# Kernel optimization log

Hardware: AMD Instinct MI355X
Metric: run time of the kernel (lower is better)

The kernel has to match this reference:

```python
import jax, jax.numpy as jnp
import numpy as np
import math

B, S, D_IN, D_OUT, H = 2, 2048, 1024, 1024, 16
HD = D_OUT // H


def setup_inputs() -> dict:
    key = jax.random.key(0)
    ks = jax.random.split(key, 6)
    scale = 0.02
    return {
        "x": jax.random.normal(ks[0], (B, S, D_IN), dtype=jnp.float32),
        "Wq": jax.random.normal(ks[1], (D_IN, D_OUT), dtype=jnp.float32) * scale,
        "Wk": jax.random.normal(ks[2], (D_IN, D_OUT), dtype=jnp.float32) * scale,
        "Wv": jax.random.normal(ks[3], (D_IN, D_OUT), dtype=jnp.float32) * scale,
        "Wo": jax.random.normal(ks[4], (D_OUT, D_OUT), dtype=jnp.float32) * scale,
        "bo": jax.random.normal(ks[5], (D_OUT,), dtype=jnp.float32) * scale,
    }


def reference(x, Wq, Wk, Wv, Wo, bo):
    b, n, _ = x.shape
    # project and split heads -> [b, h, n, hd]
    q = (x @ Wq).reshape(b, n, H, HD).transpose(0, 2, 1, 3)
    k = (x @ Wk).reshape(b, n, H, HD).transpose(0, 2, 1, 3)
    v = (x @ Wv).reshape(b, n, H, HD).transpose(0, 2, 1, 3)
    # materialized [b, h, n, n] scores with causal mask (as in original)
    scores = jnp.einsum('bhqd,bhkd->bhqk', q, k)
    causal = jnp.tril(jnp.ones((n, n), dtype=bool))  # True = keep
    scores = jnp.where(causal, scores, -jnp.inf)
    attn = jax.nn.softmax(scores / math.sqrt(HD), axis=-1)
    ctx = jnp.einsum('bhqk,bhkd->bhqd', attn, v)
    ctx = ctx.transpose(0, 2, 1, 3).reshape(b, n, D_OUT)
    return ctx @ Wo + bo
```

## Files before the change

### kernel.cpp

```cpp
#include <hip/hip_runtime.h>
#include <hip/hip_bf16.h>
#include <math.h>

typedef __bf16 v8bf __attribute__((ext_vector_type(8)));
typedef float  v4f  __attribute__((ext_vector_type(4)));
typedef unsigned short u16;

static_assert(sizeof(v8bf) == 16, "v8bf must be 16B");

__device__ __forceinline__ u16 f2bf(float f) {
  __hip_bfloat16 h = __float2bfloat16(f);
  return *reinterpret_cast<u16*>(&h);
}
__device__ __forceinline__ v4f mfma16(v8bf a, v8bf b, v4f c) {
  return __builtin_amdgcn_mfma_f32_16x16x32_bf16(a, b, c, 0, 0, 0);
}
__device__ __forceinline__ void async16(const u16* g, u16* l) {
  __builtin_amdgcn_global_load_lds(
      (__attribute__((address_space(1))) void*)(void*)g,
      (__attribute__((address_space(3))) void*)l, 16, 0, 0);
}

__global__ void convert_x(const float* __restrict__ x, u16* __restrict__ xb) {
  int i = (blockIdx.x * 256 + threadIdx.x) * 4;
  float4 v = *(const float4*)(x + i);
  ushort4 o;
  o.x = f2bf(v.x); o.y = f2bf(v.y); o.z = f2bf(v.z); o.w = f2bf(v.w);
  *(ushort4*)(xb + i) = o;
}

__global__ void transpose_w(const float* __restrict__ Wq, const float* __restrict__ Wk,
                            const float* __restrict__ Wv, const float* __restrict__ Wo,
                            u16* __restrict__ Wt) {
  __shared__ float tile[32][33];
  const float* src = (blockIdx.z == 0) ? Wq : (blockIdx.z == 1) ? Wk : (blockIdx.z == 2) ? Wv : Wo;
  int k0 = blockIdx.x * 32, n0 = blockIdx.y * 32;
  int tx = threadIdx.x, ty = threadIdx.y;
  tile[ty][tx] = src[(size_t)(k0 + ty) * 1024 + n0 + tx];
  __syncthreads();
  Wt[(size_t)(blockIdx.z * 1024 + n0 + ty) * 1024 + k0 + tx] = f2bf(tile[tx][ty]);
}

__global__ void transpose_v(const u16* __restrict__ qkv, u16* __restrict__ Vt) {
  __shared__ u16 tile[32][33];
  int b = blockIdx.z;
  int s0 = blockIdx.x * 32, d0 = blockIdx.y * 32;
  int tx = threadIdx.x, ty = threadIdx.y;
  tile[ty][tx] = qkv[(size_t)(b * 2048 + s0 + ty) * 3072 + 2048 + d0 + tx];
  __syncthreads();
  Vt[(size_t)(b * 1024 + d0 + ty) * 2048 + s0 + tx] = tile[tx][ty];
}

__device__ __forceinline__ void gemm_core(const u16* __restrict__ A, const u16* __restrict__ Bt,
                                          u16* sA, u16* sB, v4f acc[4][4], int bm, int bn) {
  const int t = threadIdx.x;
  const int w = t >> 6, l = t & 63;
  const int quad = l >> 4, low = l & 15;
  const int wm = (w & 1) * 64, wn = (w >> 1) * 64;
  const int rowA = bm * 128 + w * 32 + (l >> 2);
  const int rowB = bn * 128 + w * 32 + (l >> 2);
  const int col8 = (l & 3) * 8;
  u16* la = sA + w * 1024;
  u16* lb = sB + w * 1024;

  for (int kb = 0; kb < 1024; kb += 32) {
    async16(A + (size_t)rowA * 1024 + kb + col8, la);
    async16(A + (size_t)(rowA + 16) * 1024 + kb + col8, la + 512);
    async16(Bt + (size_t)rowB * 1024 + kb + col8, lb);
    async16(Bt + (size_t)(rowB + 16) * 1024 + kb + col8, lb + 512);
    __syncthreads();
    v8bf af[4], bfr[4];
#pragma unroll
    for (int i = 0; i < 4; i++)
      af[i] = *(const v8bf*)(sA + (wm + i * 16 + low) * 32 + quad * 8);
#pragma unroll
    for (int j = 0; j < 4; j++)
      bfr[j] = *(const v8bf*)(sB + (wn + j * 16 + low) * 32 + quad * 8);
#pragma unroll
    for (int i = 0; i < 4; i++)
#pragma unroll
      for (int j = 0; j < 4; j++)
        acc[i][j] = mfma16(af[i], bfr[j], acc[i][j]);
    __syncthreads();
  }
}

__global__ __launch_bounds__(256) void gemm_qkv(const u16* __restrict__ xb,
                                                const u16* __restrict__ Wt,
                                                u16* __restrict__ qkv) {
  __shared__ __align__(16) u16 sA[128 * 32];
  __shared__ __align__(16) u16 sB[128 * 32];
  v4f acc[4][4] = {};
  const int bm = blockIdx.x, bn = blockIdx.y;
  gemm_core(xb, Wt, sA, sB, acc, bm, bn);
  const int t = threadIdx.x, w = t >> 6, l = t & 63, quad = l >> 4, low = l & 15;
  const int wm = (w & 1) * 64, wn = (w >> 1) * 64;
#pragma unroll
  for (int i = 0; i < 4; i++) {
    int m0 = bm * 128 + wm + i * 16 + quad * 4;
#pragma unroll
    for (int j = 0; j < 4; j++) {
      int n = bn * 128 + wn + j * 16 + low;
      float qsc = (n < 1024) ? 0.18033688011112042f : 1.0f;
#pragma unroll
      for (int r = 0; r < 4; r++)
        qkv[(size_t)(m0 + r) * 3072 + n] = f2bf(acc[i][j][r] * qsc);
    }
  }
}

__global__ __launch_bounds__(256) void gemm_out(const u16* __restrict__ ctx,
                                                const u16* __restrict__ Wt,
                                                const float* __restrict__ bo,
                                                float* __restrict__ out) {
  __shared__ __align__(16) u16 sA[128 * 32];
  __shared__ __align__(16) u16 sB[64 * 32];
  const u16* Bt = Wt + (size_t)3072 * 1024;
  v4f acc[4][2] = {};
  const int bm = blockIdx.x, bn = blockIdx.y;
  const int t = threadIdx.x, w = t >> 6, l = t & 63, quad = l >> 4, low = l & 15;
  const int wm = (w & 1) * 64, wn = (w >> 1) * 32;
  const int rowA = bm * 128 + w * 32 + (l >> 2);
  const int rowB = bn * 64 + w * 16 + (l >> 2);
  const int col8 = (l & 3) * 8;
  u16* la = sA + w * 1024;
  u16* lb = sB + w * 512;

  for (int kb = 0; kb < 1024; kb += 32) {
    async16(ctx + (size_t)rowA * 1024 + kb + col8, la);
    async16(ctx + (size_t)(rowA + 16) * 1024 + kb + col8, la + 512);
    async16(Bt + (size_t)rowB * 1024 + kb + col8, lb);
    __syncthreads();
    v8bf af[4], bfr[2];
#pragma unroll
    for (int i = 0; i < 4; i++)
      af[i] = *(const v8bf*)(sA + (wm + i * 16 + low) * 32 + quad * 8);
#pragma unroll
    for (int j = 0; j < 2; j++)
      bfr[j] = *(const v8bf*)(sB + (wn + j * 16 + low) * 32 + quad * 8);
#pragma unroll
    for (int i = 0; i < 4; i++)
#pragma unroll
      for (int j = 0; j < 2; j++)
        acc[i][j] = mfma16(af[i], bfr[j], acc[i][j]);
    __syncthreads();
  }
#pragma unroll
  for (int i = 0; i < 4; i++) {
    int m0 = bm * 128 + wm + i * 16 + quad * 4;
#pragma unroll
    for (int j = 0; j < 2; j++) {
      int n = bn * 64 + wn + j * 16 + low;
      float bias = bo[n];
#pragma unroll
      for (int r = 0; r < 4; r++)
        out[(size_t)(m0 + r) * 1024 + n] = acc[i][j][r] + bias;
    }
  }
}

__global__ __launch_bounds__(256) void attn(const u16* __restrict__ qkv,
                                            const u16* __restrict__ Vt,
                                            u16* __restrict__ ctx) {
  __shared__ __align__(16) u16 sK[2][4096];
  __shared__ __align__(16) u16 sV[2][4096];
  __shared__ __align__(16) u16 pS[4][16][72];
  const int t = threadIdx.x, w = t >> 6, l = t & 63, quad = l >> 4, low = l & 15;
  const int h = blockIdx.x, tile = 31 - blockIdx.y, b = blockIdx.z;
  const int qw = tile * 64 + w * 16;
  const int nkt = tile + 1;

  const u16* kbase = qkv + (size_t)(b * 2048) * 3072 + 1024 + h * 64;
  const u16* vbase = Vt + (size_t)(b * 1024 + h * 64) * 2048;

  const int srow = l >> 3;
  const int cg = (l & 7) ^ srow;

  const u16* qrow = qkv + (size_t)(b * 2048 + qw + low) * 3072 + h * 64;
  v8bf qa0 = *(const v8bf*)(qrow + quad * 8);
  v8bf qa1 = *(const v8bf*)(qrow + 32 + quad * 8);

  float li[4] = {0.f, 0.f, 0.f, 0.f};
  v4f o[4] = {};

  {
    const u16* kg = kbase + (size_t)(w * 8 + srow) * 3072 + cg * 8;
    async16(kg, &sK[0][w * 512]);
    async16(kg + (size_t)32 * 3072, &sK[0][2048 + w * 512]);
    const u16* vg = vbase + (size_t)(w * 8 + srow) * 2048 + cg * 8;
    async16(vg, &sV[0][w * 512]);
    async16(vg + (size_t)32 * 2048, &sV[0][2048 + w * 512]);
  }

  for (int it = 0; it < nkt; it++) {
    __syncthreads();
    const int kb = it * 64;
    const int cur = it & 1;
    if (it + 1 < nkt) {
      const int nb = (it + 1) & 1;
      const u16* kg = kbase + (size_t)(kb + 64 + w * 8 + srow) * 3072 + cg * 8;
      async16(kg, &sK[nb][w * 512]);
      async16(kg + (size_t)32 * 3072, &sK[nb][2048 + w * 512]);
      const u16* vg = vbase + (size_t)(w * 8 + srow) * 2048 + kb + 64 + cg * 8;
      async16(vg, &sV[nb][w * 512]);
      async16(vg + (size_t)32 * 2048, &sV[nb][2048 + w * 512]);
    }

    v4f s[4] = {};
#pragma unroll
    for (int cf = 0; cf < 4; cf++) {
      const int key = cf * 16 + low;
#pragma unroll
      for (int ks = 0; ks < 2; ks++) {
        const int chunk = ks * 4 + quad;
        v8bf kf = *(const v8bf*)(&sK[cur][key * 64 + ((chunk ^ (key & 7)) * 8)]);
        s[cf] = mfma16(ks == 0 ? qa0 : qa1, kf, s[cf]);
      }
    }

    const bool diag = (it == nkt - 1);
#pragma unroll
    for (int r = 0; r < 4; r++) {
      const int qr = qw + quad * 4 + r;
#pragma unroll
      for (int cf = 0; cf < 4; cf++) {
        float e = __builtin_amdgcn_exp2f(s[cf][r]);
        if (diag && (kb + cf * 16 + low > qr)) e = 0.f;
        li[r] += e;
        pS[w][quad * 4 + r][cf * 16 + low] = f2bf(e);
      }
    }

    v8bf pa0 = *(const v8bf*)(&pS[w][low][quad * 8]);
    v8bf pa1 = *(const v8bf*)(&pS[w][low][32 + quad * 8]);
#pragma unroll
    for (int df = 0; df < 4; df++) {
      const int d = df * 16 + low;
      v8bf vf0 = *(const v8bf*)(&sV[cur][d * 64 + ((quad ^ (d & 7)) * 8)]);
      v8bf vf1 = *(const v8bf*)(&sV[cur][d * 64 + (((4 + quad) ^ (d & 7)) * 8)]);
      o[df] = mfma16(pa0, vf0, o[df]);
      o[df] = mfma16(pa1, vf1, o[df]);
    }
  }

#pragma unroll
  for (int off = 1; off < 16; off <<= 1)
#pragma unroll
    for (int r = 0; r < 4; r++)
      li[r] += __shfl_xor(li[r], off);

#pragma unroll
  for (int r = 0; r < 4; r++) {
    float inv = 1.f / li[r];
    int row = b * 2048 + qw + quad * 4 + r;
#pragma unroll
    for (int df = 0; df < 4; df++)
      ctx[(size_t)row * 1024 + h * 64 + df * 16 + low] = f2bf(o[df][r] * inv);
  }
}

extern "C" void kernel_launch(void* const* d_in, const int* in_sizes, int n_in,
                              void* d_out, int out_size, void* d_ws, size_t ws_size,
                              hipStream_t stream) {
  const float* x  = (const float*)d_in[0];
  const float* Wq = (const float*)d_in[1];
  const float* Wk = (const float*)d_in[2];
  const float* Wv = (const float*)d_in[3];
  const float* Wo = (const float*)d_in[4];
  const float* bo = (const float*)d_in[5];
  float* out = (float*)d_out;

  char* ws = (char*)d_ws;
  u16* xb  = (u16*)(ws);
  u16* Wt  = (u16*)(ws + 8ull * 1024 * 1024);
  u16* qkv = (u16*)(ws + 16ull * 1024 * 1024);
  u16* Vt  = (u16*)(ws + 40ull * 1024 * 1024);
  u16* ctx = (u16*)(ws + 48ull * 1024 * 1024);

  convert_x<<<dim3(4096, 1, 1), dim3(256, 1, 1), 0, stream>>>(x, xb);
  transpose_w<<<dim3(32, 32, 4), dim3(32, 32, 1), 0, stream>>>(Wq, Wk, Wv, Wo, Wt);
  gemm_qkv<<<dim3(32, 24, 1), dim3(256, 1, 1), 0, stream>>>(xb, Wt, qkv);
  transpose_v<<<dim3(64, 32, 2), dim3(32, 32, 1), 0, stream>>>(qkv, Vt);
  attn<<<dim3(16, 32, 2), dim3(256, 1, 1), 0, stream>>>(qkv, Vt, ctx);
  gemm_out<<<dim3(32, 16, 1), dim3(256, 1, 1), 0, stream>>>(ctx, Wt, bo, out);
}
```

Measured before the change: 185.4 us.

## Fuse prep kernels, write V transposed from QKV GEMM, enlarge attention query tile

Merges the x conversion and weight transposes into one prep launch. The QKV GEMM epilogue now writes separate Q, K and transposed V buffers, which removes the transpose_v kernel and a round-trip of V through memory. The attention kernel gives each wave 32 query rows (128 per block) so each K/V tile loaded into shared memory is reused twice as much, and waves skip key tiles above their causal limit. The cost is fewer blocks, which may leave CUs idle, more registers per thread, and strided column writes for Vt that are poorly coalesced.

```diff
diff --git a/kernel.cpp b/kernel.cpp
--- a/kernel.cpp
+++ b/kernel.cpp
@@ -21,34 +21,26 @@
       (__attribute__((address_space(3))) void*)l, 16, 0, 0);
 }
 
-__global__ void convert_x(const float* __restrict__ x, u16* __restrict__ xb) {
-  int i = (blockIdx.x * 256 + threadIdx.x) * 4;
-  float4 v = *(const float4*)(x + i);
-  ushort4 o;
-  o.x = f2bf(v.x); o.y = f2bf(v.y); o.z = f2bf(v.z); o.w = f2bf(v.w);
-  *(ushort4*)(xb + i) = o;
-}
-
-__global__ void transpose_w(const float* __restrict__ Wq, const float* __restrict__ Wk,
-                            const float* __restrict__ Wv, const float* __restrict__ Wo,
-                            u16* __restrict__ Wt) {
+__global__ void prep(const float* __restrict__ x, const float* __restrict__ Wq,
+                     const float* __restrict__ Wk, const float* __restrict__ Wv,
+                     const float* __restrict__ Wo, u16* __restrict__ Wt,
+                     u16* __restrict__ xb) {
+  int tx = threadIdx.x, ty = threadIdx.y;
+  if (blockIdx.z == 4) {
+    int bid = blockIdx.y * 32 + blockIdx.x;
+    int i = (bid * 1024 + ty * 32 + tx) * 4;
+    float4 v = *(const float4*)(x + i);
+    ushort4 o;
+    o.x = f2bf(v.x); o.y = f2bf(v.y); o.z = f2bf(v.z); o.w = f2bf(v.w);
+    *(ushort4*)(xb + i) = o;
+    return;
+  }
   __shared__ float tile[32][33];
   const float* src = (blockIdx.z == 0) ? Wq : (blockIdx.z == 1) ? Wk : (blockIdx.z == 2) ? Wv : Wo;
   int k0 = blockIdx.x * 32, n0 = blockIdx.y * 32;
-  int tx = threadIdx.x, ty = threadIdx.y;
   tile[ty][tx] = src[(size_t)(k0 + ty) * 1024 + n0 + tx];
   __syncthreads();
   Wt[(size_t)(blockIdx.z * 1024 + n0 + ty) * 1024 + k0 + tx] = f2bf(tile[tx][ty]);
-}
-
-__global__ void transpose_v(const u16* __restrict__ qkv, u16* __restrict__ Vt) {
-  __shared__ u16 tile[32][33];
-  int b = blockIdx.z;
-  int s0 = blockIdx.x * 32, d0 = blockIdx.y * 32;
-  int tx = threadIdx.x, ty = threadIdx.y;
-  tile[ty][tx] = qkv[(size_t)(b * 2048 + s0 + ty) * 3072 + 2048 + d0 + tx];
-  __syncthreads();
-  Vt[(size_t)(b * 1024 + d0 + ty) * 2048 + s0 + tx] = tile[tx][ty];
 }
 
 __device__ __forceinline__ void gemm_core(const u16* __restrict__ A, const u16* __restrict__ Bt,
@@ -87,7 +79,9 @@
 
 __global__ __launch_bounds__(256) void gemm_qkv(const u16* __restrict__ xb,
                                                 const u16* __restrict__ Wt,
-                                                u16* __restrict__ qkv) {
+                                                u16* __restrict__ Qb,
+                                                u16* __restrict__ Kb,
+                                                u16* __restrict__ Vt) {
   __shared__ __align__(16) u16 sA[128 * 32];
   __shared__ __align__(16) u16 sB[128 * 32];
   v4f acc[4][4] = {};
@@ -95,16 +89,28 @@
   gemm_core(xb, Wt, sA, sB, acc, bm, bn);
   const int t = threadIdx.x, w = t >> 6, l = t & 63, quad = l >> 4, low = l & 15;
   const int wm = (w & 1) * 64, wn = (w >> 1) * 64;
+  const int zone = (bn * 128) >> 10;
+  const float qsc = (zone == 0) ? 0.18033688011112042f : 1.0f;
 #pragma unroll
   for (int i = 0; i < 4; i++) {
     int m0 = bm * 128 + wm + i * 16 + quad * 4;
 #pragma unroll
     for (int j = 0; j < 4; j++) {
-      int n = bn * 128 + wn + j * 16 + low;
-      float qsc = (n < 1024) ? 0.18033688011112042f : 1.0f;
-#pragma unroll
-      for (int r = 0; r < 4; r++)
-        qkv[(size_t)(m0 + r) * 3072 + n] = f2bf(acc[i][j][r] * qsc);
+      int nn = (bn * 128 + wn + j * 16 + low) & 1023;
+      if (zone == 0) {
+#pragma unroll
+        for (int r = 0; r < 4; r++)
+          Qb[(size_t)(m0 + r) * 1024 + nn] = f2bf(acc[i][j][r] * qsc);
+      } else if (zone == 1) {
+#pragma unroll
+        for (int r = 0; r < 4; r++)
+          Kb[(size_t)(m0 + r) * 1024 + nn] = f2bf(acc[i][j][r]);
+      } else {
+        int bb = m0 >> 11, s = m0 & 2047;
+#pragma unroll
+        for (int r = 0; r < 4; r++)
+          Vt[(size_t)(bb * 1024 + nn) * 2048 + s + r] = f2bf(acc[i][j][r]);
+      }
     }
   }
 }
@@ -159,34 +165,39 @@
   }
 }
 
-__global__ __launch_bounds__(256) void attn(const u16* __restrict__ qkv,
+__global__ __launch_bounds__(256) void attn(const u16* __restrict__ Qb,
+                                            const u16* __restrict__ Kb,
                                             const u16* __restrict__ Vt,
                                             u16* __restrict__ ctx) {
   __shared__ __align__(16) u16 sK[2][4096];
   __shared__ __align__(16) u16 sV[2][4096];
-  __shared__ __align__(16) u16 pS[4][16][72];
+  __shared__ __align__(16) u16 pS[4][32][72];
   const int t = threadIdx.x, w = t >> 6, l = t & 63, quad = l >> 4, low = l & 15;
-  const int h = blockIdx.x, tile = 31 - blockIdx.y, b = blockIdx.z;
-  const int qw = tile * 64 + w * 16;
-  const int nkt = tile + 1;
-
-  const u16* kbase = qkv + (size_t)(b * 2048) * 3072 + 1024 + h * 64;
+  const int h = blockIdx.x, tile = 15 - blockIdx.y, b = blockIdx.z;
+  const int qw = tile * 128 + w * 32;
+  const int nkt = 2 * tile + 2;
+
+  const u16* kbase = Kb + (size_t)(b * 2048) * 1024 + h * 64;
   const u16* vbase = Vt + (size_t)(b * 1024 + h * 64) * 2048;
 
   const int srow = l >> 3;
   const int cg = (l & 7) ^ srow;
 
-  const u16* qrow = qkv + (size_t)(b * 2048 + qw + low) * 3072 + h * 64;
-  v8bf qa0 = *(const v8bf*)(qrow + quad * 8);
-  v8bf qa1 = *(const v8bf*)(qrow + 32 + quad * 8);
-
-  float li[4] = {0.f, 0.f, 0.f, 0.f};
-  v4f o[4] = {};
+  v8bf qa[2][2];
+#pragma unroll
+  for (int mi = 0; mi < 2; mi++) {
+    const u16* qrow = Qb + (size_t)(b * 2048 + qw + mi * 16 + low) * 1024 + h * 64;
+    qa[mi][0] = *(const v8bf*)(qrow + quad * 8);
+    qa[mi][1] = *(const v8bf*)(qrow + 32 + quad * 8);
+  }
+
+  float li[2][4] = {};
+  v4f o[2][4] = {};
 
   {
-    const u16* kg = kbase + (size_t)(w * 8 + srow) * 3072 + cg * 8;
+    const u16* kg = kbase + (size_t)(w * 8 + srow) * 1024 + cg * 8;
     async16(kg, &sK[0][w * 512]);
-    async16(kg + (size_t)32 * 3072, &sK[0][2048 + w * 512]);
+    async16(kg + (size_t)32 * 1024, &sK[0][2048 + w * 512]);
     const u16* vg = vbase + (size_t)(w * 8 + srow) * 2048 + cg * 8;
     async16(vg, &sV[0][w * 512]);
     async16(vg + (size_t)32 * 2048, &sV[0][2048 + w * 512]);
@@ -198,65 +209,82 @@
     const int cur = it & 1;
     if (it + 1 < nkt) {
       const int nb = (it + 1) & 1;
-      const u16* kg = kbase + (size_t)(kb + 64 + w * 8 + srow) * 3072 + cg * 8;
+      const u16* kg = kbase + (size_t)(kb + 64 + w * 8 + srow) * 1024 + cg * 8;
       async16(kg, &sK[nb][w * 512]);
-      async16(kg + (size_t)32 * 3072, &sK[nb][2048 + w * 512]);
+      async16(kg + (size_t)32 * 1024, &sK[nb][2048 + w * 512]);
       const u16* vg = vbase + (size_t)(w * 8 + srow) * 2048 + kb + 64 + cg * 8;
       async16(vg, &sV[nb][w * 512]);
       async16(vg + (size_t)32 * 2048, &sV[nb][2048 + w * 512]);
     }
 
-    v4f s[4] = {};
-#pragma unroll
-    for (int cf = 0; cf < 4; cf++) {
-      const int key = cf * 16 + low;
-#pragma unroll
-      for (int ks = 0; ks < 2; ks++) {
-        const int chunk = ks * 4 + quad;
-        v8bf kf = *(const v8bf*)(&sK[cur][key * 64 + ((chunk ^ (key & 7)) * 8)]);
-        s[cf] = mfma16(ks == 0 ? qa0 : qa1, kf, s[cf]);
+    const bool active = (kb <= qw + 31);
+    if (active) {
+      v4f s[2][4] = {};
+#pragma unroll
+      for (int cf = 0; cf < 4; cf++) {
+        const int key = cf * 16 + low;
+        v8bf kf0 = *(const v8bf*)(&sK[cur][key * 64 + ((quad ^ (key & 7)) * 8)]);
+        v8bf kf1 = *(const v8bf*)(&sK[cur][key * 64 + (((4 + quad) ^ (key & 7)) * 8)]);
+#pragma unroll
+        for (int mi = 0; mi < 2; mi++) {
+          s[mi][cf] = mfma16(qa[mi][0], kf0, s[mi][cf]);
+          s[mi][cf] = mfma16(qa[mi][1], kf1, s[mi][cf]);
+        }
       }
-    }
-
-    const bool diag = (it == nkt - 1);
+
+      const bool dm = (kb + 63 > qw);
+#pragma unroll
+      for (int mi = 0; mi < 2; mi++)
+#pragma unroll
+        for (int r = 0; r < 4; r++) {
+          const int qr = qw + mi * 16 + quad * 4 + r;
+#pragma unroll
+          for (int cf = 0; cf < 4; cf++) {
+            float e = __builtin_amdgcn_exp2f(s[mi][cf][r]);
+            if (dm && (kb + cf * 16 + low > qr)) e = 0.f;
+            li[mi][r] += e;
+            pS[w][mi * 16 + quad * 4 + r][cf * 16 + low] = f2bf(e);
+          }
+        }
+
+      v8bf pa[2][2];
+#pragma unroll
+      for (int mi = 0; mi < 2; mi++) {
+        pa[mi][0] = *(const v8bf*)(&pS[w][mi * 16 + low][quad * 8]);
+        pa[mi][1] = *(const v8bf*)(&pS[w][mi * 16 + low][32 + quad * 8]);
+      }
+#pragma unroll
+      for (int df = 0; df < 4; df++) {
+        const int d = df * 16 + low;
+        v8bf vf0 = *(const v8bf*)(&sV[cur][d * 64 + ((quad ^ (d & 7)) * 8)]);
+        v8bf vf1 = *(const v8bf*)(&sV[cur][d * 64 + (((4 + quad) ^ (d & 7)) * 8)]);
+#pragma unroll
+        for (int mi = 0; mi < 2; mi++) {
+          o[mi][df] = mfma16(pa[mi][0], vf0, o[mi][df]);
+          o[mi][df] = mfma16(pa[mi][1], vf1, o[mi][df]);
+        }
+      }
+    }
+  }
+
+#pragma unroll
+  for (int off = 1; off < 16; off <<= 1)
+#pragma unroll
+    for (int mi = 0; mi < 2; mi++)
+#pragma unroll
+      for (int r = 0; r < 4; r++)
+        li[mi][r] += __shfl_xor(li[mi][r], off);
+
+#pragma unroll
+  for (int mi = 0; mi < 2; mi++)
 #pragma unroll
     for (int r = 0; r < 4; r++) {
-      const int qr = qw + quad * 4 + r;
-#pragma unroll
-      for (int cf = 0; cf < 4; cf++) {
-        float e = __builtin_amdgcn_exp2f(s[cf][r]);
-        if (diag && (kb + cf * 16 + low > qr)) e = 0.f;
-        li[r] += e;
-        pS[w][quad * 4 + r][cf * 16 + low] = f2bf(e);
-      }
-    }
-
-    v8bf pa0 = *(const v8bf*)(&pS[w][low][quad * 8]);
-    v8bf pa1 = *(const v8bf*)(&pS[w][low][32 + quad * 8]);
-#pragma unroll
-    for (int df = 0; df < 4; df++) {
-      const int d = df * 16 + low;
-      v8bf vf0 = *(const v8bf*)(&sV[cur][d * 64 + ((quad ^ (d & 7)) * 8)]);
-      v8bf vf1 = *(const v8bf*)(&sV[cur][d * 64 + (((4 + quad) ^ (d & 7)) * 8)]);
-      o[df] = mfma16(pa0, vf0, o[df]);
-      o[df] = mfma16(pa1, vf1, o[df]);
-    }
-  }
-
-#pragma unroll
-  for (int off = 1; off < 16; off <<= 1)
-#pragma unroll
-    for (int r = 0; r < 4; r++)
-      li[r] += __shfl_xor(li[r], off);
-
-#pragma unroll
-  for (int r = 0; r < 4; r++) {
-    float inv = 1.f / li[r];
-    int row = b * 2048 + qw + quad * 4 + r;
-#pragma unroll
-    for (int df = 0; df < 4; df++)
-      ctx[(size_t)row * 1024 + h * 64 + df * 16 + low] = f2bf(o[df][r] * inv);
-  }
+      float inv = 1.f / li[mi][r];
+      int row = b * 2048 + qw + mi * 16 + quad * 4 + r;
+#pragma unroll
+      for (int df = 0; df < 4; df++)
+        ctx[(size_t)row * 1024 + h * 64 + df * 16 + low] = f2bf(o[mi][df][r] * inv);
+    }
 }
 
 extern "C" void kernel_launch(void* const* d_in, const int* in_sizes, int n_in,
@@ -273,14 +301,13 @@
   char* ws = (char*)d_ws;
   u16* xb  = (u16*)(ws);
   u16* Wt  = (u16*)(ws + 8ull * 1024 * 1024);
-  u16* qkv = (u16*)(ws + 16ull * 1024 * 1024);
-  u16* Vt  = (u16*)(ws + 40ull * 1024 * 1024);
-  u16* ctx = (u16*)(ws + 48ull * 1024 * 1024);
-
-  convert_x<<<dim3(4096, 1, 1), dim3(256, 1, 1), 0, stream>>>(x, xb);
-  transpose_w<<<dim3(32, 32, 4), dim3(32, 32, 1), 0, stream>>>(Wq, Wk, Wv, Wo, Wt);
-  gemm_qkv<<<dim3(32, 24, 1), dim3(256, 1, 1), 0, stream>>>(xb, Wt, qkv);
-  transpose_v<<<dim3(64, 32, 2), dim3(32, 32, 1), 0, stream>>>(qkv, Vt);
-  attn<<<dim3(16, 32, 2), dim3(256, 1, 1), 0, stream>>>(qkv, Vt, ctx);
+  u16* Qb  = (u16*)(ws + 16ull * 1024 * 1024);
+  u16* Kb  = (u16*)(ws + 24ull * 1024 * 1024);
+  u16* Vt  = (u16*)(ws + 32ull * 1024 * 1024);
+  u16* ctx = (u16*)(ws + 40ull * 1024 * 1024);
+
+  prep<<<dim3(32, 32, 5), dim3(32, 32, 1), 0, stream>>>(x, Wq, Wk, Wv, Wo, Wt, xb);
+  gemm_qkv<<<dim3(32, 24, 1), dim3(256, 1, 1), 0, stream>>>(xb, Wt, Qb, Kb, Vt);
+  attn<<<dim3(16, 16, 2), dim3(256, 1, 1), 0, stream>>>(Qb, Kb, Vt, ctx);
   gemm_out<<<dim3(32, 16, 1), dim3(256, 1, 1), 0, stream>>>(ctx, Wt, bo, out);
 }
```

New measurement: 205.5 us. 10.8% more time.
